# Optimization experiments

Hardware: AMD Instinct MI355X
Metric: run time of the kernel (lower is better)

Reference implementation:

```python
import jax, jax.numpy as jnp
import numpy as np


def log_g(x):
    # log of g(x) = where(x>=0, x+0.5, sigmoid(x)), computed stably in log space
    return jnp.where(x >= 0, jnp.log(jax.nn.relu(x) + 0.5), -jax.nn.softplus(-x))


def setup_inputs() -> dict:
    key = jax.random.key(0)
    k1, k2, k3, k4 = jax.random.split(key, 4)
    B, S, D, Di = 4, 8192, 512, 1024
    X = jax.random.normal(k1, (B, S, D), dtype=jnp.float32)
    # prev_hidden must be strictly positive (its log is taken)
    hidden = jax.random.uniform(k2, (B, 1, Di), dtype=jnp.float32) * 0.9 + 0.1
    W_hg = jax.random.normal(k3, (2 * Di, D), dtype=jnp.float32) * 0.02
    W_out = jax.random.normal(k4, (D, Di), dtype=jnp.float32) * 0.02
    return {"X": X, "hidden": hidden, "W_hg": W_hg, "W_out": W_out}


def reference(X, hidden, W_hg, W_out):
    # X: [B,S,D]; hidden: [B,1,Di]; W_hg: [2Di,D]; W_out: [D,Di]
    S = X.shape[1]
    hg = jnp.einsum('bsd,ed->bse', X, W_hg)            # [B,S,2Di]
    h, gate = jnp.split(hg, 2, axis=-1)                # each [B,S,Di]

    log_coeffs = -jax.nn.softplus(gate)                # log(1 - z)
    log_z = -jax.nn.softplus(-gate)                    # log z
    log_values = log_z + log_g(h)                      # log(z * g(h_tilde))

    # prepend prev hidden state
    log_values = jnp.concatenate([jnp.log(hidden), log_values], axis=1)  # [B,S+1,Di]
    log_coeffs = jnp.pad(log_coeffs, ((0, 0), (1, 0), (0, 0)))           # [B,S+1,Di]

    # Heinsen associative scan in log space
    a_star = jnp.cumsum(log_coeffs, axis=1)
    log_h = a_star + jax.lax.cumlogsumexp(log_values - a_star, axis=1)
    h_all = jnp.exp(log_h)[:, -S:]                     # [B,S,Di]

    next_prev_hidden = h_all[:, -1:]                   # [B,1,Di]
    out = jnp.einsum('bsi,di->bsd', h_all, W_out)      # [B,S,D]
    return out, next_prev_hidden
```

## Files before the change

### kernel.cpp

```cpp
#include <hip/hip_runtime.h>
#include <hip/hip_bf16.h>
#include <stdint.h>

typedef __attribute__((ext_vector_type(8))) short short8;
typedef __attribute__((ext_vector_type(4))) float f32x4;

#define CH 64
#define NC 128

__device__ __forceinline__ unsigned short f2bf(float f) {
  union { float f; unsigned u; } x; x.f = f;
  unsigned u = x.u;
  u = (u + 0x7fffu + ((u >> 16) & 1u)) >> 16;
  return (unsigned short)u;
}
__device__ __forceinline__ float bf2f(unsigned u16) {
  union { unsigned u; float f; } x; x.u = u16 << 16;
  return x.f;
}

#define GLOAD_LDS16(gptr, lptr) \
  __builtin_amdgcn_global_load_lds((const __attribute__((address_space(1))) void*)(gptr), \
                                   (__attribute__((address_space(3))) void*)(lptr), 16, 0, 0)

__global__ void k_f32_to_bf16(const float* __restrict__ src, unsigned short* __restrict__ dst, int n4) {
  int i = blockIdx.x * blockDim.x + threadIdx.x;
  if (i >= n4) return;
  float4 f = reinterpret_cast<const float4*>(src)[i];
  ushort4 o = make_ushort4(f2bf(f.x), f2bf(f.y), f2bf(f.z), f2bf(f.w));
  reinterpret_cast<ushort4*>(dst)[i] = o;
}

__global__ __launch_bounds__(256, 2) void k_gemm1(
    const unsigned short* __restrict__ Xb,
    const unsigned short* __restrict__ Wb,
    uint32_t* __restrict__ avArr,
    float* __restrict__ Acar, float* __restrict__ Vcar)
{
  __shared__ unsigned short As[128 * 64];
  __shared__ unsigned short Bs0[128 * 64];
  __shared__ unsigned short Bs1[128 * 64];

  const int m0 = blockIdx.y * 128;
  const int i0 = blockIdx.x * 128;
  const int tid = threadIdx.x;
  const int lane = tid & 63;
  const int wave = tid >> 6;
  const int wm = (wave >> 1) * 64;
  const int wn = (wave & 1) * 64;
  const int srow = tid >> 3;
  const int scol = (tid & 7) * 8;

  f32x4 acc0[4][4], acc1[4][4];
#pragma unroll
  for (int f = 0; f < 4; ++f)
#pragma unroll
    for (int g = 0; g < 4; ++g) {
      acc0[f][g] = f32x4{0.f, 0.f, 0.f, 0.f};
      acc1[f][g] = f32x4{0.f, 0.f, 0.f, 0.f};
    }

  for (int k0 = 0; k0 < 512; k0 += 64) {
    __syncthreads();
#pragma unroll
    for (int j = 0; j < 4; ++j) {
      int row = j * 32 + srow;
      GLOAD_LDS16(Xb + (size_t)(m0 + row) * 512 + k0 + scol, As + row * 64 + scol);
    }
#pragma unroll
    for (int j = 0; j < 4; ++j) {
      int row = j * 32 + srow;
      GLOAD_LDS16(Wb + (size_t)(i0 + row) * 512 + k0 + scol, Bs0 + row * 64 + scol);
    }
#pragma unroll
    for (int j = 0; j < 4; ++j) {
      int row = j * 32 + srow;
      GLOAD_LDS16(Wb + (size_t)(1024 + i0 + row) * 512 + k0 + scol, Bs1 + row * 64 + scol);
    }
    __syncthreads();

#pragma unroll
    for (int kk = 0; kk < 2; ++kk) {
      const int kof = kk * 32 + (lane >> 4) * 8;
      const int rl = lane & 15;
      short8 av[4], b0[4], b1[4];
#pragma unroll
      for (int f = 0; f < 4; ++f)
        av[f] = *(const short8*)(As + (wm + f * 16 + rl) * 64 + kof);
#pragma unroll
      for (int g = 0; g < 4; ++g) {
        b0[g] = *(const short8*)(Bs0 + (wn + g * 16 + rl) * 64 + kof);
        b1[g] = *(const short8*)(Bs1 + (wn + g * 16 + rl) * 64 + kof);
      }
#pragma unroll
      for (int f = 0; f < 4; ++f)
#pragma unroll
        for (int g = 0; g < 4; ++g) {
          acc0[f][g] = __builtin_amdgcn_mfma_f32_16x16x32_bf16(av[f], b0[g], acc0[f][g], 0, 0, 0);
          acc1[f][g] = __builtin_amdgcn_mfma_f32_16x16x32_bf16(av[f], b1[g], acc1[f][g], 0, 0, 0);
        }
    }
  }

  const int rl = lane & 15;
  const int q  = lane >> 4;
  const int mb = m0 + wm;
  const int b  = mb >> 13;
  const int c  = (mb & 8191) >> 6;

#pragma unroll
  for (int g = 0; g < 4; ++g) {
    const int i = i0 + wn + g * 16 + rl;
    float Achunk = 1.f, Vchunk = 0.f;
#pragma unroll
    for (int f = 0; f < 4; ++f) {
      float Aseg = 1.f, Vseg = 0.f;
#pragma unroll
      for (int r = 0; r < 4; ++r) {
        float h    = acc0[f][g][r];
        float gate = acc1[f][g][r];
        float e  = __expf(gate);
        float ac = __builtin_amdgcn_rcpf(1.f + e);
        float z  = e * ac;
        float gg;
        if (h >= 0.f) gg = h + 0.5f;
        else { float eh = __expf(h); gg = eh * __builtin_amdgcn_rcpf(1.f + eh); }
        float v = z * gg;
        int m = mb + f * 16 + q * 4 + r;
        avArr[(size_t)m * 1024 + i] = (uint32_t)f2bf(ac) | ((uint32_t)f2bf(v) << 16);
        Vseg = Vseg * ac + v;
        Aseg = Aseg * ac;
      }
      {
        float Ap = __shfl_xor(Aseg, 16);
        float Vp = __shfl_xor(Vseg, 16);
        if (q & 1) { Vseg = Vp * Aseg + Vseg; Aseg = Ap * Aseg; }
        else       { Vseg = Vseg * Ap + Vp;   Aseg = Aseg * Ap; }
      }
      {
        float Ap = __shfl_xor(Aseg, 32);
        float Vp = __shfl_xor(Vseg, 32);
        if (q & 2) { Vseg = Vp * Aseg + Vseg; Aseg = Ap * Aseg; }
        else       { Vseg = Vseg * Ap + Vp;   Aseg = Aseg * Ap; }
      }
      Vchunk = Vchunk * Aseg + Vseg;
      Achunk = Achunk * Aseg;
    }
    if (lane < 16) {
      size_t co = ((size_t)b * NC + c) * 1024 + i;
      Acar[co] = Achunk;
      Vcar[co] = Vchunk;
    }
  }
}

__global__ void k_scanB(const float* __restrict__ hidden,
                        const float* __restrict__ Acar, const float* __restrict__ Vcar,
                        float* __restrict__ Hstart)
{
  int t = blockIdx.x * blockDim.x + threadIdx.x;
  int b = t >> 10, i = t & 1023;
  float H = hidden[(size_t)b * 1024 + i];
  for (int c = 0; c < NC; ++c) {
    size_t o = ((size_t)b * NC + c) * 1024 + i;
    Hstart[o] = H;
    H = fmaf(Acar[o], H, Vcar[o]);
  }
}

__global__ void k_scanC(const uint32_t* __restrict__ av,
                        const float* __restrict__ Hstart,
                        unsigned short* __restrict__ hAll, float* __restrict__ nextH)
{
  int c = blockIdx.x & (NC - 1);
  int b = blockIdx.x >> 7;
  size_t base4 = (((size_t)b * 8192 + (size_t)c * CH) * 1024) / 4 + threadIdx.x;
  size_t ho = (((size_t)b * NC + c) * 1024) / 4 + threadIdx.x;
  float4 H = reinterpret_cast<const float4*>(Hstart)[ho];
#pragma unroll 4
  for (int t = 0; t < CH; ++t) {
    uint4 u = reinterpret_cast<const uint4*>(av)[base4 + (size_t)t * 256];
    H.x = fmaf(bf2f(u.x & 0xffffu), H.x, bf2f(u.x >> 16));
    H.y = fmaf(bf2f(u.y & 0xffffu), H.y, bf2f(u.y >> 16));
    H.z = fmaf(bf2f(u.z & 0xffffu), H.z, bf2f(u.z >> 16));
    H.w = fmaf(bf2f(u.w & 0xffffu), H.w, bf2f(u.w >> 16));
    ushort4 o = make_ushort4(f2bf(H.x), f2bf(H.y), f2bf(H.z), f2bf(H.w));
    reinterpret_cast<ushort4*>(hAll)[base4 + (size_t)t * 256] = o;
  }
  if (c == NC - 1)
    reinterpret_cast<float4*>(nextH)[(size_t)b * 256 + threadIdx.x] = H;
}

__global__ __launch_bounds__(256, 2) void k_gemm2(
    const unsigned short* __restrict__ Ab,
    const unsigned short* __restrict__ Bb,
    float* __restrict__ out)
{
  __shared__ unsigned short As[128 * 64];
  __shared__ unsigned short Bs[128 * 64];

  const int m0 = blockIdx.y * 128;
  const int n0 = blockIdx.x * 128;
  const int tid = threadIdx.x;
  const int lane = tid & 63;
  const int wave = tid >> 6;
  const int wm = (wave >> 1) * 64;
  const int wn = (wave & 1) * 64;
  const int srow = tid >> 3;
  const int scol = (tid & 7) * 8;

  f32x4 acc[4][4];
#pragma unroll
  for (int f = 0; f < 4; ++f)
#pragma unroll
    for (int g = 0; g < 4; ++g) acc[f][g] = f32x4{0.f, 0.f, 0.f, 0.f};

  for (int k0 = 0; k0 < 1024; k0 += 64) {
    __syncthreads();
#pragma unroll
    for (int j = 0; j < 4; ++j) {
      int row = j * 32 + srow;
      GLOAD_LDS16(Ab + (size_t)(m0 + row) * 1024 + k0 + scol, As + row * 64 + scol);
    }
#pragma unroll
    for (int j = 0; j < 4; ++j) {
      int row = j * 32 + srow;
      GLOAD_LDS16(Bb + (size_t)(n0 + row) * 1024 + k0 + scol, Bs + row * 64 + scol);
    }
    __syncthreads();

#pragma unroll
    for (int kk = 0; kk < 2; ++kk) {
      const int kof = kk * 32 + (lane >> 4) * 8;
      const int rl = lane & 15;
      short8 av[4], bv[4];
#pragma unroll
      for (int f = 0; f < 4; ++f)
        av[f] = *(const short8*)(As + (wm + f * 16 + rl) * 64 + kof);
#pragma unroll
      for (int g = 0; g < 4; ++g)
        bv[g] = *(const short8*)(Bs + (wn + g * 16 + rl) * 64 + kof);
#pragma unroll
      for (int f = 0; f < 4; ++f)
#pragma unroll
        for (int g = 0; g < 4; ++g)
          acc[f][g] = __builtin_amdgcn_mfma_f32_16x16x32_bf16(av[f], bv[g], acc[f][g], 0, 0, 0);
    }
  }

  const int rl = lane & 15;
  const int rr = (lane >> 4) * 4;
#pragma unroll
  for (int f = 0; f < 4; ++f)
#pragma unroll
    for (int g = 0; g < 4; ++g)
#pragma unroll
      for (int r = 0; r < 4; ++r) {
        int m = m0 + wm + f * 16 + rr + r;
        int n = n0 + wn + g * 16 + rl;
        out[(size_t)m * 512 + n] = acc[f][g][r];
      }
}

extern "C" void kernel_launch(void* const* d_in, const int* in_sizes, int n_in,
                              void* d_out, int out_size, void* d_ws, size_t ws_size,
                              hipStream_t stream) {
  const float* X      = (const float*)d_in[0];
  const float* hidden = (const float*)d_in[1];
  const float* W_hg   = (const float*)d_in[2];
  const float* W_out  = (const float*)d_in[3];

  float* out   = (float*)d_out;
  float* nextH = out + (size_t)32768 * 512;

  char* ws = (char*)d_ws;
  size_t off = 0;
  auto alloc = [&](size_t bytes) -> void* {
    void* p = ws + off;
    off = (off + bytes + 255) & ~(size_t)255;
    return p;
  };
  unsigned short* Xb    = (unsigned short*)alloc(32768ULL * 512 * 2);
  unsigned short* Whgb  = (unsigned short*)alloc(2048ULL * 512 * 2);
  unsigned short* Woutb = (unsigned short*)alloc(512ULL * 1024 * 2);
  unsigned short* hAll  = (unsigned short*)alloc(32768ULL * 1024 * 2);
  float*    Acar   = (float*)alloc(4ULL * NC * 1024 * 4);
  float*    Vcar   = (float*)alloc(4ULL * NC * 1024 * 4);
  float*    Hstart = (float*)alloc(4ULL * NC * 1024 * 4);
  uint32_t* avArr  = (uint32_t*)alloc(32768ULL * 1024 * 4);

  k_f32_to_bf16<<<16384, 256, 0, stream>>>(X, Xb, 16777216 / 4);
  k_f32_to_bf16<<<1024, 256, 0, stream>>>(W_hg, Whgb, 1048576 / 4);
  k_f32_to_bf16<<<512, 256, 0, stream>>>(W_out, Woutb, 524288 / 4);

  dim3 g1(8, 256);
  k_gemm1<<<g1, 256, 0, stream>>>(Xb, Whgb, avArr, Acar, Vcar);

  k_scanB<<<16, 256, 0, stream>>>(hidden, Acar, Vcar, Hstart);
  k_scanC<<<4 * NC, 256, 0, stream>>>(avArr, Hstart, hAll, nextH);

  dim3 g2(4, 256);
  k_gemm2<<<g2, 256, 0, stream>>>(hAll, Woutb, out);
}
```

Before: 329.4 us.

## Fuse chunk scan into output GEMM via LDS and merge conversion kernels

The per-chunk scan now writes its bf16 hidden states into a 128KB swizzled LDS tile, and the same block then runs the output GEMM from LDS. This removes the hAll round trip through global memory and one kernel launch. The three f32-to-bf16 conversions are also merged into one launch. In exchange, LDS use is large, so occupancy is low (at most one block per CU despite the launch bounds), only 512 blocks run, and W_out is read directly from global/L2 without staging.

```diff
diff --git a/kernel.cpp b/kernel.cpp
--- a/kernel.cpp
+++ b/kernel.cpp
@@ -23,12 +23,21 @@
   __builtin_amdgcn_global_load_lds((const __attribute__((address_space(1))) void*)(gptr), \
                                    (__attribute__((address_space(3))) void*)(lptr), 16, 0, 0)
 
-__global__ void k_f32_to_bf16(const float* __restrict__ src, unsigned short* __restrict__ dst, int n4) {
+#define NQ_X   4194304
+#define NQ_WHG  262144
+#define NQ_WOUT 131072
+__global__ void k_cvt_all(const float* __restrict__ X, const float* __restrict__ Whg,
+                          const float* __restrict__ Wout,
+                          unsigned short* __restrict__ Xb, unsigned short* __restrict__ Whgb,
+                          unsigned short* __restrict__ Woutb) {
   int i = blockIdx.x * blockDim.x + threadIdx.x;
-  if (i >= n4) return;
-  float4 f = reinterpret_cast<const float4*>(src)[i];
+  const float* src; unsigned short* dst; int off;
+  if (i < NQ_X)                { src = X;    dst = Xb;    off = i; }
+  else if (i < NQ_X + NQ_WHG)  { src = Whg;  dst = Whgb;  off = i - NQ_X; }
+  else                         { src = Wout; dst = Woutb; off = i - NQ_X - NQ_WHG; }
+  float4 f = reinterpret_cast<const float4*>(src)[off];
   ushort4 o = make_ushort4(f2bf(f.x), f2bf(f.y), f2bf(f.z), f2bf(f.w));
-  reinterpret_cast<ushort4*>(dst)[i] = o;
+  reinterpret_cast<ushort4*>(dst)[off] = o;
 }
 
 __global__ __launch_bounds__(256, 2) void k_gemm1(
@@ -168,96 +177,81 @@
   }
 }
 
-__global__ void k_scanC(const uint32_t* __restrict__ av,
-                        const float* __restrict__ Hstart,
-                        unsigned short* __restrict__ hAll, float* __restrict__ nextH)
+__global__ __launch_bounds__(512, 2) void k_scan_gemm2(
+    const uint32_t* __restrict__ av,
+    const float* __restrict__ Hstart,
+    const unsigned short* __restrict__ Wout,
+    float* __restrict__ out,
+    float* __restrict__ nextH)
 {
-  int c = blockIdx.x & (NC - 1);
-  int b = blockIdx.x >> 7;
-  size_t base4 = (((size_t)b * 8192 + (size_t)c * CH) * 1024) / 4 + threadIdx.x;
-  size_t ho = (((size_t)b * NC + c) * 1024) / 4 + threadIdx.x;
-  float4 H = reinterpret_cast<const float4*>(Hstart)[ho];
+  __shared__ unsigned short hs[64 * 1024];
+
+  const int chunk = blockIdx.x;
+  const int b = chunk >> 7;
+  const int c = chunk & 127;
+  const int mb = b * 8192 + c * 64;
+  const int tid = threadIdx.x;
+
+  {
+    const int i2 = tid * 2;
+    float2 H = reinterpret_cast<const float2*>(Hstart + ((size_t)(b * NC + c)) * 1024)[tid];
+    const uint2* av2 = reinterpret_cast<const uint2*>(av) + (size_t)mb * 512 + tid;
 #pragma unroll 4
-  for (int t = 0; t < CH; ++t) {
-    uint4 u = reinterpret_cast<const uint4*>(av)[base4 + (size_t)t * 256];
-    H.x = fmaf(bf2f(u.x & 0xffffu), H.x, bf2f(u.x >> 16));
-    H.y = fmaf(bf2f(u.y & 0xffffu), H.y, bf2f(u.y >> 16));
-    H.z = fmaf(bf2f(u.z & 0xffffu), H.z, bf2f(u.z >> 16));
-    H.w = fmaf(bf2f(u.w & 0xffffu), H.w, bf2f(u.w >> 16));
-    ushort4 o = make_ushort4(f2bf(H.x), f2bf(H.y), f2bf(H.z), f2bf(H.w));
-    reinterpret_cast<ushort4*>(hAll)[base4 + (size_t)t * 256] = o;
-  }
-  if (c == NC - 1)
-    reinterpret_cast<float4*>(nextH)[(size_t)b * 256 + threadIdx.x] = H;
-}
-
-__global__ __launch_bounds__(256, 2) void k_gemm2(
-    const unsigned short* __restrict__ Ab,
-    const unsigned short* __restrict__ Bb,
-    float* __restrict__ out)
-{
-  __shared__ unsigned short As[128 * 64];
-  __shared__ unsigned short Bs[128 * 64];
-
-  const int m0 = blockIdx.y * 128;
-  const int n0 = blockIdx.x * 128;
-  const int tid = threadIdx.x;
+    for (int t = 0; t < CH; ++t) {
+      uint2 u = av2[(size_t)t * 512];
+      H.x = fmaf(bf2f(u.x & 0xffffu), H.x, bf2f(u.x >> 16));
+      H.y = fmaf(bf2f(u.y & 0xffffu), H.y, bf2f(u.y >> 16));
+      uint32_t packed = (uint32_t)f2bf(H.x) | ((uint32_t)f2bf(H.y) << 16);
+      int byte = (t * 2048 + i2 * 2) ^ ((t & 7) << 4);
+      *reinterpret_cast<uint32_t*>(reinterpret_cast<char*>(hs) + byte) = packed;
+    }
+    if (c == NC - 1)
+      reinterpret_cast<float2*>(nextH + (size_t)b * 1024)[tid] = H;
+  }
+  __syncthreads();
+
   const int lane = tid & 63;
   const int wave = tid >> 6;
-  const int wm = (wave >> 1) * 64;
-  const int wn = (wave & 1) * 64;
-  const int srow = tid >> 3;
-  const int scol = (tid & 7) * 8;
-
-  f32x4 acc[4][4];
-#pragma unroll
-  for (int f = 0; f < 4; ++f)
-#pragma unroll
-    for (int g = 0; g < 4; ++g) acc[f][g] = f32x4{0.f, 0.f, 0.f, 0.f};
-
-  for (int k0 = 0; k0 < 1024; k0 += 64) {
-    __syncthreads();
-#pragma unroll
-    for (int j = 0; j < 4; ++j) {
-      int row = j * 32 + srow;
-      GLOAD_LDS16(Ab + (size_t)(m0 + row) * 1024 + k0 + scol, As + row * 64 + scol);
-    }
-#pragma unroll
-    for (int j = 0; j < 4; ++j) {
-      int row = j * 32 + srow;
-      GLOAD_LDS16(Bb + (size_t)(n0 + row) * 1024 + k0 + scol, Bs + row * 64 + scol);
-    }
-    __syncthreads();
-
-#pragma unroll
-    for (int kk = 0; kk < 2; ++kk) {
-      const int kof = kk * 32 + (lane >> 4) * 8;
-      const int rl = lane & 15;
-      short8 av[4], bv[4];
-#pragma unroll
-      for (int f = 0; f < 4; ++f)
-        av[f] = *(const short8*)(As + (wm + f * 16 + rl) * 64 + kof);
-#pragma unroll
-      for (int g = 0; g < 4; ++g)
-        bv[g] = *(const short8*)(Bs + (wn + g * 16 + rl) * 64 + kof);
-#pragma unroll
-      for (int f = 0; f < 4; ++f)
-#pragma unroll
-        for (int g = 0; g < 4; ++g)
-          acc[f][g] = __builtin_amdgcn_mfma_f32_16x16x32_bf16(av[f], bv[g], acc[f][g], 0, 0, 0);
-    }
-  }
-
+  const int wm2 = (wave >> 2) * 32;
+  const int wn2 = (wave & 3) * 128;
   const int rl = lane & 15;
-  const int rr = (lane >> 4) * 4;
-#pragma unroll
-  for (int f = 0; f < 4; ++f)
-#pragma unroll
-    for (int g = 0; g < 4; ++g)
+  const int q  = lane >> 4;
+
+  f32x4 acc[2][8];
+#pragma unroll
+  for (int f = 0; f < 2; ++f)
+#pragma unroll
+    for (int g = 0; g < 8; ++g) acc[f][g] = f32x4{0.f, 0.f, 0.f, 0.f};
+
+  for (int kk = 0; kk < 32; ++kk) {
+    const int kof = kk * 32 + q * 8;
+    short8 a[2], bv[8];
+#pragma unroll
+    for (int f = 0; f < 2; ++f) {
+      int row = wm2 + f * 16 + rl;
+      int byte = (row * 2048 + kof * 2) ^ ((row & 7) << 4);
+      a[f] = *reinterpret_cast<const short8*>(reinterpret_cast<const char*>(hs) + byte);
+    }
+#pragma unroll
+    for (int g = 0; g < 8; ++g) {
+      int n = wn2 + g * 16 + rl;
+      bv[g] = *reinterpret_cast<const short8*>(Wout + (size_t)n * 1024 + kof);
+    }
+#pragma unroll
+    for (int f = 0; f < 2; ++f)
+#pragma unroll
+      for (int g = 0; g < 8; ++g)
+        acc[f][g] = __builtin_amdgcn_mfma_f32_16x16x32_bf16(a[f], bv[g], acc[f][g], 0, 0, 0);
+  }
+
+#pragma unroll
+  for (int f = 0; f < 2; ++f)
+#pragma unroll
+    for (int g = 0; g < 8; ++g)
 #pragma unroll
       for (int r = 0; r < 4; ++r) {
-        int m = m0 + wm + f * 16 + rr + r;
-        int n = n0 + wn + g * 16 + rl;
+        int m = mb + wm2 + f * 16 + q * 4 + r;
+        int n = wn2 + g * 16 + rl;
         out[(size_t)m * 512 + n] = acc[f][g][r];
       }
 }
@@ -283,22 +277,17 @@
   unsigned short* Xb    = (unsigned short*)alloc(32768ULL * 512 * 2);
   unsigned short* Whgb  = (unsigned short*)alloc(2048ULL * 512 * 2);
   unsigned short* Woutb = (unsigned short*)alloc(512ULL * 1024 * 2);
-  unsigned short* hAll  = (unsigned short*)alloc(32768ULL * 1024 * 2);
   float*    Acar   = (float*)alloc(4ULL * NC * 1024 * 4);
   float*    Vcar   = (float*)alloc(4ULL * NC * 1024 * 4);
   float*    Hstart = (float*)alloc(4ULL * NC * 1024 * 4);
   uint32_t* avArr  = (uint32_t*)alloc(32768ULL * 1024 * 4);
 
-  k_f32_to_bf16<<<16384, 256, 0, stream>>>(X, Xb, 16777216 / 4);
-  k_f32_to_bf16<<<1024, 256, 0, stream>>>(W_hg, Whgb, 1048576 / 4);
-  k_f32_to_bf16<<<512, 256, 0, stream>>>(W_out, Woutb, 524288 / 4);
+  k_cvt_all<<<17920, 256, 0, stream>>>(X, W_hg, W_out, Xb, Whgb, Woutb);
 
   dim3 g1(8, 256);
   k_gemm1<<<g1, 256, 0, stream>>>(Xb, Whgb, avArr, Acar, Vcar);
 
   k_scanB<<<16, 256, 0, stream>>>(hidden, Acar, Vcar, Hstart);
-  k_scanC<<<4 * NC, 256, 0, stream>>>(avArr, Hstart, hAll, nextH);
-
-  dim3 g2(4, 256);
-  k_gemm2<<<g2, 256, 0, stream>>>(hAll, Woutb, out);
-}
+
+  k_scan_gemm2<<<512, 512, 0, stream>>>(avArr, Hstart, Woutb, out, nextH);
+}
```

After: 381.9 us. 1.16x slower.
